# Kernel optimization log

Hardware: AMD Instinct MI355X
Metric: run time of the kernel (lower is better)

The kernel has to match this reference:

```python
import jax, jax.numpy as jnp
import numpy as np

N_NODES, N_EDGES = 50000, 800000
IN_DIM, OUT_DIM, EDGE_DIM = 128, 128, 32
NUM_HEADS = 8
HEAD_DIM = OUT_DIM // NUM_HEADS
SCALE = HEAD_DIM ** -0.5


def setup_inputs() -> dict:
    key = jax.random.key(0)
    ks = jax.random.split(key, 8)
    def lin_w(k, fan_in, fan_out):
        # kaiming-uniform-ish init like nn.Linear
        bound = 1.0 / np.sqrt(fan_in)
        return jax.random.uniform(k, (fan_in, fan_out), jnp.float32, -bound, bound)
    return {
        "node_features": jax.random.normal(ks[0], (N_NODES, IN_DIM), jnp.float32),
        "edge_features": jax.random.normal(ks[1], (N_EDGES, EDGE_DIM), jnp.float32),
        "Wq": lin_w(ks[2], IN_DIM, OUT_DIM), "bq": jnp.zeros((OUT_DIM,), jnp.float32),
        "Wk": lin_w(ks[3], IN_DIM, OUT_DIM), "bk": jnp.zeros((OUT_DIM,), jnp.float32),
        "Wv": lin_w(ks[4], IN_DIM, OUT_DIM), "bv": jnp.zeros((OUT_DIM,), jnp.float32),
        "We": lin_w(ks[5], EDGE_DIM, OUT_DIM), "be": jnp.zeros((OUT_DIM,), jnp.float32),
        "edge_list": jax.random.randint(ks[6], (N_EDGES, 2), 0, N_NODES, jnp.int32),
        "num_nodes": N_NODES,
    }


def reference(node_features, edge_features, Wq, bq, Wk, bk, Wv, bv, We, be, edge_list, num_nodes):
    # node projections -> [N, H, D]
    Q = (node_features @ Wq + bq).reshape(-1, NUM_HEADS, HEAD_DIM)
    K = (node_features @ Wk + bk).reshape(-1, NUM_HEADS, HEAD_DIM)
    V = (node_features @ Wv + bv).reshape(-1, NUM_HEADS, HEAD_DIM)
    edge_bias = (edge_features @ We + be).reshape(-1, NUM_HEADS, HEAD_DIM)

    src = edge_list[:, 0]  # node_in
    dst = edge_list[:, 1]  # node_out

    # per-edge per-head scores: [E, H]
    scores = jnp.einsum("ehd,ehd->eh", Q[src], K[dst]) * SCALE + edge_bias.sum(-1)
    # NOTE: softmax over the HEADS axis (dim=1), exactly as in the source
    weights = jax.nn.softmax(scores, axis=1)

    # weighted messages gathered from src, scattered to dst: [E, H, D] -> [N, H, D]
    msg = V[src] * weights[..., None]
    node_updates = jax.ops.segment_sum(msg, dst, num_segments=num_nodes)
    return node_updates.reshape(num_nodes, OUT_DIM)
```

## Files before the change

kernel.cpp:

```cpp
#include <hip/hip_runtime.h>
#include <math.h>

#define IN_DIM   128
#define OUT_DIM  128
#define EDGE_DIM 32
#define NUM_HEADS 8
#define HEAD_DIM 16
#define SCALE 0.25f
#define CSTRIDE 16

typedef __attribute__((ext_vector_type(8))) short bf16x8;
typedef __attribute__((ext_vector_type(4))) float f32x4;
typedef __attribute__((ext_vector_type(4))) unsigned int u32x4;

__device__ inline unsigned short f2bf(float x) {
    unsigned int u = __float_as_uint(x);
    unsigned int r = u + 0x7fff + ((u >> 16) & 1);
    return (unsigned short)(r >> 16);
}
__device__ inline float bflo(unsigned int u) { return __uint_as_float(u << 16); }
__device__ inline float bfhi(unsigned int u) { return __uint_as_float(u & 0xffff0000u); }

__global__ __launch_bounds__(256) void setup_kernel(
    int* __restrict__ counts, int n_nodes, int nbz,
    const float* __restrict__ Wq, const float* __restrict__ Wk,
    const float* __restrict__ Wv, unsigned short* __restrict__ WtB, int nbw,
    const float* __restrict__ We, const float* __restrict__ be,
    float* __restrict__ WeR, float* __restrict__ beR,
    const float* __restrict__ X, unsigned short* __restrict__ Xb)
{
    const int bx = blockIdx.x;
    const int t  = threadIdx.x;
    if (bx < nbz) {
        const int i = bx * 256 + t;
        if (i < n_nodes) counts[i << 4] = 0;
    } else if (bx < nbz + nbw) {
        const int idx = (bx - nbz) * 256 + t;
        const int mat = idx >> 14;
        const int rem = idx & 16383;
        const int n = rem >> 7, k = rem & 127;
        const float* W = (mat == 0) ? Wq : (mat == 1) ? Wk : Wv;
        WtB[mat * 16384 + n * 128 + k] = f2bf(W[k * 128 + n]);
    } else if (bx == nbz + nbw) {
        const int k = t >> 3, h = t & 7;
        float s = 0.f;
#pragma unroll
        for (int d = 0; d < HEAD_DIM; ++d) s += We[k * OUT_DIM + h * HEAD_DIM + d];
        WeR[k * NUM_HEADS + h] = s;
        if (t < NUM_HEADS) {
            float sb = 0.f;
#pragma unroll
            for (int d = 0; d < HEAD_DIM; ++d) sb += be[t * HEAD_DIM + d];
            beR[t] = sb;
        }
    } else {
        const int i = (bx - (nbz + nbw + 1)) * 256 + t;
        if (i < n_nodes * 16) {
            const f32x4* xr = (const f32x4*)(X + (size_t)i * 8);
            const f32x4 x0 = xr[0], x1 = xr[1];
            u32x4 p;
            p[0] = (unsigned)f2bf(x0[0]) | ((unsigned)f2bf(x0[1]) << 16);
            p[1] = (unsigned)f2bf(x0[2]) | ((unsigned)f2bf(x0[3]) << 16);
            p[2] = (unsigned)f2bf(x1[0]) | ((unsigned)f2bf(x1[1]) << 16);
            p[3] = (unsigned)f2bf(x1[2]) | ((unsigned)f2bf(x1[3]) << 16);
            *(u32x4*)(Xb + (size_t)i * 8) = p;
        }
    }
}

__global__ __launch_bounds__(256) void edge_kernel(
    const int* __restrict__ el, int* __restrict__ counts, int* __restrict__ rank,
    const float* __restrict__ ef, const float* __restrict__ WeR,
    const float* __restrict__ beR, unsigned int* __restrict__ ebias_e,
    int n_edges)
{
    const int e = blockIdx.x * 256 + threadIdx.x;
    if (e >= n_edges) return;
    const int2 ed = ((const int2*)el)[e];
    rank[e] = atomicAdd(&counts[ed.y << 4], 1);

    float acc[NUM_HEADS];
#pragma unroll
    for (int h = 0; h < NUM_HEADS; ++h) acc[h] = beR[h];

    const f32x4* efr = (const f32x4*)(ef + (size_t)e * EDGE_DIM);
#pragma unroll
    for (int kk = 0; kk < 8; ++kk) {
        const f32x4 f = efr[kk];
#pragma unroll
        for (int c = 0; c < 4; ++c) {
            const float* wr = WeR + (kk * 4 + c) * NUM_HEADS;
#pragma unroll
            for (int h = 0; h < NUM_HEADS; ++h)
                acc[h] = fmaf(f[c], wr[h], acc[h]);
        }
    }
    u32x4 pk;
    pk[0] = (unsigned)f2bf(acc[0]) | ((unsigned)f2bf(acc[1]) << 16);
    pk[1] = (unsigned)f2bf(acc[2]) | ((unsigned)f2bf(acc[3]) << 16);
    pk[2] = (unsigned)f2bf(acc[4]) | ((unsigned)f2bf(acc[5]) << 16);
    pk[3] = (unsigned)f2bf(acc[6]) | ((unsigned)f2bf(acc[7]) << 16);
    *(u32x4*)(ebias_e + (size_t)e * 4) = pk;
}

__global__ __launch_bounds__(256) void qkv_kernel(
    const unsigned short* __restrict__ Xb, const unsigned short* __restrict__ WtB,
    const float* __restrict__ bq, const float* __restrict__ bk,
    const float* __restrict__ bv,
    unsigned short* __restrict__ QVb, unsigned short* __restrict__ Kb,
    int n_nodes, int nbm)
{
    __shared__ unsigned short shW[16384];
    const int bx = blockIdx.x;
    const int t  = threadIdx.x;

    const int which = bx / nbm;
    const int mb    = bx - which * nbm;
    const unsigned short* Wg = WtB + which * 16384;

#pragma unroll
    for (int kk = 0; kk < 8; ++kk) {
        const int c = kk * 256 + t;
        const u32x4 v = ((const u32x4*)Wg)[c];
        const int row = c >> 4;
        const int bir = (c & 15) << 4;
        *(u32x4*)((char*)shW + row * 256 + (bir ^ ((row & 7) << 4))) = v;
    }
    __syncthreads();

    const int wave = t >> 6, lane = t & 63;
    const int quad = lane >> 4, li = lane & 15;
    const int mbase = mb * 256 + wave * 64;

    int mrow[4];
#pragma unroll
    for (int m = 0; m < 4; ++m) {
        const int r_ = mbase + m * 16 + li;
        mrow[m] = (r_ < n_nodes) ? r_ : (n_nodes - 1);
    }

    f32x4 acc[4][8];
#pragma unroll
    for (int m = 0; m < 4; ++m)
#pragma unroll
        for (int nt = 0; nt < 8; ++nt) acc[m][nt] = (f32x4){0.f, 0.f, 0.f, 0.f};

#pragma unroll
    for (int ks = 0; ks < 4; ++ks) {
        bf16x8 a[4];
#pragma unroll
        for (int m = 0; m < 4; ++m)
            a[m] = *(const bf16x8*)(Xb + (size_t)mrow[m] * 128 + ks * 32 + quad * 8);
#pragma unroll
        for (int nt = 0; nt < 8; ++nt) {
            const int row = nt * 16 + li;
            const bf16x8 b = *(const bf16x8*)((const char*)shW + row * 256 +
                                ((ks * 64 + quad * 16) ^ ((row & 7) << 4)));
#pragma unroll
            for (int m = 0; m < 4; ++m)
                acc[m][nt] = __builtin_amdgcn_mfma_f32_16x16x32_bf16(a[m], b, acc[m][nt], 0, 0, 0);
        }
    }

    const float* bias = (which == 0) ? bq : (which == 1) ? bk : bv;
    float bv8[8];
#pragma unroll
    for (int nt = 0; nt < 8; ++nt) bv8[nt] = bias[nt * 16 + li];

    __syncthreads();

    unsigned short* stg = shW + wave * 2176;
    const int R = lane >> 2, cc4 = lane & 3;
#pragma unroll
    for (int m = 0; m < 4; ++m) {
#pragma unroll
        for (int nt = 0; nt < 8; ++nt)
#pragma unroll
            for (int r = 0; r < 4; ++r)
                stg[(quad * 4 + r) * 136 + nt * 16 + li] = f2bf(acc[m][nt][r] + bv8[nt]);
        __syncthreads();

        const int node = mbase + m * 16 + R;
        if (node < n_nodes) {
            const u32x4* s = (const u32x4*)(stg + R * 136 + cc4 * 32);
            u32x4 d0 = s[0], d1 = s[1], d2 = s[2], d3 = s[3];
            unsigned short* dp =
                (which == 0) ? (QVb + (size_t)node * 256 + cc4 * 32)
              : (which == 1) ? (Kb  + (size_t)node * 128 + cc4 * 32)
              :                (QVb + (size_t)node * 256 + 128 + cc4 * 32);
            u32x4* d = (u32x4*)dp;
            d[0] = d0; d[1] = d1; d[2] = d2; d[3] = d3;
        }
        __syncthreads();
    }
}

__global__ __launch_bounds__(256) void scan1_kernel(
    const int* __restrict__ counts, int* __restrict__ bsums, int n)
{
    __shared__ int lds[256];
    const int i = blockIdx.x * 256 + threadIdx.x;
    lds[threadIdx.x] = (i < n) ? counts[i << 4] : 0;
    __syncthreads();
    for (int off = 128; off > 0; off >>= 1) {
        if (threadIdx.x < off) lds[threadIdx.x] += lds[threadIdx.x + off];
        __syncthreads();
    }
    if (threadIdx.x == 0) bsums[blockIdx.x] = lds[0];
}

__global__ __launch_bounds__(256) void scan3_kernel(
    const int* __restrict__ counts, const int* __restrict__ bsums,
    int* __restrict__ offsets, int n, int n_edges, int nb)
{
    __shared__ int lds[256];
    const int t = threadIdx.x;

    int v = (t < nb) ? bsums[t] : 0;
    lds[t] = v;
    __syncthreads();
    for (int off = 1; off < 256; off <<= 1) {
        const int u = (t >= off) ? lds[t - off] : 0;
        __syncthreads();
        lds[t] += u;
        __syncthreads();
    }
    const int base = (blockIdx.x > 0) ? lds[blockIdx.x - 1] : 0;
    __syncthreads();

    const int i = blockIdx.x * 256 + t;
    const int c = (i < n) ? counts[i << 4] : 0;
    lds[t] = c;
    __syncthreads();
    for (int off = 1; off < 256; off <<= 1) {
        const int u = (t >= off) ? lds[t - off] : 0;
        __syncthreads();
        lds[t] += u;
        __syncthreads();
    }
    if (i < n) offsets[i] = base + lds[t] - c;
    if (blockIdx.x == 0 && t == 0) offsets[n] = n_edges;
}

__global__ __launch_bounds__(256) void scatter_kernel(
    const int* __restrict__ el, const int* __restrict__ rank,
    const unsigned int* __restrict__ ebias_e,
    const int* __restrict__ offsets, unsigned int* __restrict__ recs,
    int n_edges)
{
    const int e = blockIdx.x * 256 + threadIdx.x;
    if (e >= n_edges) return;
    const int2 ed = ((const int2*)el)[e];
    const u32x4 eb = *(const u32x4*)(ebias_e + (size_t)e * 4);
    const int pos = offsets[ed.y] + rank[e];

    u32x4 r0, r1;
    r0[0] = (unsigned)ed.x;
    r0[1] = 0;
    r0[2] = eb[0];
    r0[3] = eb[1];
    r1[0] = eb[2];
    r1[1] = eb[3];
    r1[2] = 0; r1[3] = 0;
    u32x4* rp = (u32x4*)(recs + (size_t)pos * 8);
    rp[0] = r0;
    rp[1] = r1;
}

__global__ __launch_bounds__(256) void aggregate_kernel(
    const unsigned short* __restrict__ QVb, const unsigned short* __restrict__ Kb,
    const int* __restrict__ offsets, const unsigned int* __restrict__ recs,
    float* __restrict__ out, int n_nodes)
{
    const int wave = threadIdx.x >> 6;
    const int lane = threadIdx.x & 63;
    const int node = blockIdx.x * 4 + wave;
    if (node >= n_nodes) return;
    const int g = lane >> 3;
    const int h = lane & 7;

    const int beg = offsets[node];
    const int end = offsets[node + 1];
    const int cnt = end - beg;

    float kf[16];
    {
        const u32x4* kp = (const u32x4*)(Kb + (size_t)node * 128 + h * 16);
        const u32x4 ka = kp[0], kb_ = kp[1];
#pragma unroll
        for (int j = 0; j < 4; ++j) { kf[j * 2] = bflo(ka[j]);  kf[j * 2 + 1] = bfhi(ka[j]); }
#pragma unroll
        for (int j = 0; j < 4; ++j) { kf[8 + j * 2] = bflo(kb_[j]); kf[8 + j * 2 + 1] = bfhi(kb_[j]); }
    }

    float acc[16];
#pragma unroll
    for (int d = 0; d < 16; ++d) acc[d] = 0.f;

    if (cnt > 0) {
        const int last = end - 1;
        const int ebd  = 2 + (h >> 1);

        int s0 = beg + g;            if (s0 > last) s0 = last;
        unsigned int src_c = recs[(size_t)s0 * 8];
        unsigned int ebw_c = recs[(size_t)s0 * 8 + ebd];
        u32x4 qa, qb, va, vb;
        {
            const u32x4* qp = (const u32x4*)(QVb + (size_t)src_c * 256 + h * 16);
            qa = qp[0]; qb = qp[1];
            const u32x4* vp = (const u32x4*)(QVb + (size_t)src_c * 256 + 128 + h * 16);
            va = vp[0]; vb = vp[1];
        }
        int s1 = beg + 8 + g;        if (s1 > last) s1 = last;
        unsigned int src_n = recs[(size_t)s1 * 8];
        unsigned int ebw_n = recs[(size_t)s1 * 8 + ebd];

        for (int i = 0; i < cnt; i += 8) {
            int s2 = beg + i + 16 + g;  if (s2 > last) s2 = last;
            const unsigned int src_f = recs[(size_t)s2 * 8];
            const unsigned int ebw_f = recs[(size_t)s2 * 8 + ebd];
            u32x4 qan, qbn, van, vbn;
            {
                const u32x4* qp = (const u32x4*)(QVb + (size_t)src_n * 256 + h * 16);
                qan = qp[0]; qbn = qp[1];
                const u32x4* vp = (const u32x4*)(QVb + (size_t)src_n * 256 + 128 + h * 16);
                van = vp[0]; vbn = vp[1];
            }

            const float eb = (h & 1) ? bfhi(ebw_c) : bflo(ebw_c);
            float p = 0.f;
#pragma unroll
            for (int j = 0; j < 4; ++j) {
                p = fmaf(bflo(qa[j]), kf[j * 2],     p);
                p = fmaf(bfhi(qa[j]), kf[j * 2 + 1], p);
            }
#pragma unroll
            for (int j = 0; j < 4; ++j) {
                p = fmaf(bflo(qb[j]), kf[8 + j * 2],     p);
                p = fmaf(bfhi(qb[j]), kf[8 + j * 2 + 1], p);
            }
            const float score = fmaf(p, SCALE, eb);

            float mx = score;
            mx = fmaxf(mx, __shfl_xor(mx, 1));
            mx = fmaxf(mx, __shfl_xor(mx, 2));
            mx = fmaxf(mx, __shfl_xor(mx, 4));
            const float ex = __expf(score - mx);
            float den = ex;
            den += __shfl_xor(den, 1);
            den += __shfl_xor(den, 2);
            den += __shfl_xor(den, 4);
            float w = __fdividef(ex, den);
            if (i + g >= cnt) w = 0.f;

#pragma unroll
            for (int j = 0; j < 4; ++j) {
                acc[j * 2]     = fmaf(w, bflo(va[j]), acc[j * 2]);
                acc[j * 2 + 1] = fmaf(w, bfhi(va[j]), acc[j * 2 + 1]);
            }
#pragma unroll
            for (int j = 0; j < 4; ++j) {
                acc[8 + j * 2]     = fmaf(w, bflo(vb[j]), acc[8 + j * 2]);
                acc[8 + j * 2 + 1] = fmaf(w, bfhi(vb[j]), acc[8 + j * 2 + 1]);
            }

            qa = qan; qb = qbn; va = van; vb = vbn;
            src_c = src_n; ebw_c = ebw_n;
            src_n = src_f; ebw_n = ebw_f;
        }
    }

#pragma unroll
    for (int mask = 8; mask <= 32; mask <<= 1)
#pragma unroll
        for (int d = 0; d < 16; ++d)
            acc[d] += __shfl_xor(acc[d], mask);

    float2 o2 = make_float2(acc[g * 2], acc[g * 2 + 1]);
    *(float2*)(out + (size_t)node * OUT_DIM + h * 16 + g * 2) = o2;
}

extern "C" void kernel_launch(void* const* d_in, const int* in_sizes, int n_in,
                              void* d_out, int out_size, void* d_ws, size_t ws_size,
                              hipStream_t stream)
{
    const float* X   = (const float*)d_in[0];
    const float* ef  = (const float*)d_in[1];
    const float* Wq  = (const float*)d_in[2];
    const float* bq  = (const float*)d_in[3];
    const float* Wk  = (const float*)d_in[4];
    const float* bk  = (const float*)d_in[5];
    const float* Wv  = (const float*)d_in[6];
    const float* bv  = (const float*)d_in[7];
    const float* We  = (const float*)d_in[8];
    const float* be  = (const float*)d_in[9];
    const int*   el  = (const int*)d_in[10];

    const int n_nodes = in_sizes[0] / IN_DIM;
    const int n_edges = in_sizes[10] / 2;

    char* w = (char*)d_ws;
    auto alloc = [&](size_t bytes) { char* p = w; w += (bytes + 255) & ~(size_t)255; return p; };

    unsigned short* QVb    = (unsigned short*)alloc((size_t)n_nodes * 256 * 2);
    unsigned short* Kb     = (unsigned short*)alloc((size_t)n_nodes * 128 * 2);
    unsigned short* WtB    = (unsigned short*)alloc((size_t)3 * 128 * 128 * 2);
    unsigned int*   recs   = (unsigned int*)alloc((size_t)n_edges * 32);
    unsigned int*   ebias_e= (unsigned int*)alloc((size_t)n_edges * 16);
    int* rank    = (int*)alloc((size_t)n_edges * 4);
    float* WeR   = (float*)alloc(EDGE_DIM * NUM_HEADS * 4);
    float* beR   = (float*)alloc(NUM_HEADS * 4);
    int* counts  = (int*)alloc((size_t)n_nodes * CSTRIDE * 4);
    int* offsets = (int*)alloc((size_t)(n_nodes + 1) * 4);
    int* bsums   = (int*)alloc(256 * 4);

    unsigned short* Xb = (unsigned short*)recs;

    const int nbz = (n_nodes + 255) / 256;
    const int nbw = (3 * 128 * 128) / 256;
    const int nbx = (n_nodes * 16 + 255) / 256;
    setup_kernel<<<nbz + nbw + 1 + nbx, 256, 0, stream>>>(
        counts, n_nodes, nbz, Wq, Wk, Wv, WtB, nbw, We, be, WeR, beR, X, Xb);

    const int nbh = (n_edges + 255) / 256;
    edge_kernel<<<nbh, 256, 0, stream>>>(
        el, counts, rank, ef, WeR, beR, ebias_e, n_edges);

    const int nbm = (n_nodes + 255) / 256;
    qkv_kernel<<<3 * nbm, 256, 0, stream>>>(
        Xb, WtB, bq, bk, bv, QVb, Kb, n_nodes, nbm);

    const int nb = (n_nodes + 255) / 256;
    scan1_kernel<<<nb, 256, 0, stream>>>(counts, bsums, n_nodes);
    scan3_kernel<<<nb, 256, 0, stream>>>(counts, bsums, offsets, n_nodes, n_edges, nb);

    scatter_kernel<<<nbh, 256, 0, stream>>>(
        el, rank, ebias_e, offsets, recs, n_edges);

    aggregate_kernel<<<(n_nodes + 3) / 4, 256, 0, stream>>>(
        QVb, Kb, offsets, recs, (float*)d_out, n_nodes);
}
```

Measured before the change: 322.8 us.

## Make aggregate kernel persistent with packed float2 math and no softmax max

The aggregate kernel becomes a persistent grid-stride loop: the grid is capped at 2048 blocks, each wave walks over nodes, and the next node's CSR offsets are prefetched before the current node is processed. The dot-product and accumulation loops use two-wide float vectors, which the compiler can map to packed FMA instructions. The per-edge max-reduction across heads before the exponential is removed, saving three shuffles and a max per edge. Without the max subtraction, large scores could overflow the exponential, so correctness now depends on the score range.

New measurement: 326.1 us. Within noise of the previous version (+1.0%).

```diff
diff --git a/kernel.cpp b/kernel.cpp
--- a/kernel.cpp
+++ b/kernel.cpp
@@ -11,6 +11,7 @@
 
 typedef __attribute__((ext_vector_type(8))) short bf16x8;
 typedef __attribute__((ext_vector_type(4))) float f32x4;
+typedef __attribute__((ext_vector_type(2))) float f32x2;
 typedef __attribute__((ext_vector_type(4))) unsigned int u32x4;
 
 __device__ inline unsigned short f2bf(float x) {
@@ -20,6 +21,9 @@
 }
 __device__ inline float bflo(unsigned int u) { return __uint_as_float(u << 16); }
 __device__ inline float bfhi(unsigned int u) { return __uint_as_float(u & 0xffff0000u); }
+__device__ inline f32x2 up2(unsigned int u) {
+    f32x2 r; r[0] = bflo(u); r[1] = bfhi(u); return r;
+}
 
 __global__ __launch_bounds__(256) void setup_kernel(
     int* __restrict__ counts, int n_nodes, int nbz,
@@ -270,114 +274,109 @@
 __global__ __launch_bounds__(256) void aggregate_kernel(
     const unsigned short* __restrict__ QVb, const unsigned short* __restrict__ Kb,
     const int* __restrict__ offsets, const unsigned int* __restrict__ recs,
-    float* __restrict__ out, int n_nodes)
-{
-    const int wave = threadIdx.x >> 6;
+    float* __restrict__ out, int n_nodes, int nwtot)
+{
     const int lane = threadIdx.x & 63;
-    const int node = blockIdx.x * 4 + wave;
-    if (node >= n_nodes) return;
     const int g = lane >> 3;
     const int h = lane & 7;
-
-    const int beg = offsets[node];
-    const int end = offsets[node + 1];
-    const int cnt = end - beg;
-
-    float kf[16];
-    {
-        const u32x4* kp = (const u32x4*)(Kb + (size_t)node * 128 + h * 16);
-        const u32x4 ka = kp[0], kb_ = kp[1];
-#pragma unroll
-        for (int j = 0; j < 4; ++j) { kf[j * 2] = bflo(ka[j]);  kf[j * 2 + 1] = bfhi(ka[j]); }
-#pragma unroll
-        for (int j = 0; j < 4; ++j) { kf[8 + j * 2] = bflo(kb_[j]); kf[8 + j * 2 + 1] = bfhi(kb_[j]); }
-    }
-
-    float acc[16];
-#pragma unroll
-    for (int d = 0; d < 16; ++d) acc[d] = 0.f;
-
-    if (cnt > 0) {
-        const int last = end - 1;
-        const int ebd  = 2 + (h >> 1);
-
-        int s0 = beg + g;            if (s0 > last) s0 = last;
-        unsigned int src_c = recs[(size_t)s0 * 8];
-        unsigned int ebw_c = recs[(size_t)s0 * 8 + ebd];
-        u32x4 qa, qb, va, vb;
+    const int ebd = 2 + (h >> 1);
+
+    int node = (blockIdx.x * 256 + threadIdx.x) >> 6;
+    if (node >= n_nodes) return;
+    int beg = offsets[node];
+    int end = offsets[node + 1];
+
+    for (;;) {
+        const int nnode = node + nwtot;
+        int nbeg = 0, nend = 0;
+        if (nnode < n_nodes) { nbeg = offsets[nnode]; nend = offsets[nnode + 1]; }
+
+        const int cnt = end - beg;
+
+        f32x2 kf[8];
         {
-            const u32x4* qp = (const u32x4*)(QVb + (size_t)src_c * 256 + h * 16);
-            qa = qp[0]; qb = qp[1];
-            const u32x4* vp = (const u32x4*)(QVb + (size_t)src_c * 256 + 128 + h * 16);
-            va = vp[0]; vb = vp[1];
-        }
-        int s1 = beg + 8 + g;        if (s1 > last) s1 = last;
-        unsigned int src_n = recs[(size_t)s1 * 8];
-        unsigned int ebw_n = recs[(size_t)s1 * 8 + ebd];
-
-        for (int i = 0; i < cnt; i += 8) {
-            int s2 = beg + i + 16 + g;  if (s2 > last) s2 = last;
-            const unsigned int src_f = recs[(size_t)s2 * 8];
-            const unsigned int ebw_f = recs[(size_t)s2 * 8 + ebd];
-            u32x4 qan, qbn, van, vbn;
-            {
-                const u32x4* qp = (const u32x4*)(QVb + (size_t)src_n * 256 + h * 16);
-                qan = qp[0]; qbn = qp[1];
-                const u32x4* vp = (const u32x4*)(QVb + (size_t)src_n * 256 + 128 + h * 16);
-                van = vp[0]; vbn = vp[1];
+            const u32x4* kp = (const u32x4*)(Kb + (size_t)node * 128 + h * 16);
+            const u32x4 ka = kp[0], kb_ = kp[1];
+#pragma unroll
+            for (int j = 0; j < 4; ++j) { kf[j] = up2(ka[j]); kf[4 + j] = up2(kb_[j]); }
+        }
+
+        f32x2 acc[8];
+#pragma unroll
+        for (int j = 0; j < 8; ++j) acc[j] = (f32x2){0.f, 0.f};
+
+        if (cnt > 0) {
+            const int last = end - 1;
+            int s0 = beg + g; if (s0 > last) s0 = last;
+            const unsigned src_c = recs[(size_t)s0 * 8];
+            unsigned ebw_c = recs[(size_t)s0 * 8 + ebd];
+            const unsigned short* bp0 = QVb + (size_t)src_c * 256 + h * 16;
+            u32x4 qa = *(const u32x4*)bp0;
+            u32x4 qb = *(const u32x4*)(bp0 + 8);
+            u32x4 va = *(const u32x4*)(bp0 + 128);
+            u32x4 vb = *(const u32x4*)(bp0 + 136);
+            int s1 = beg + 8 + g; if (s1 > last) s1 = last;
+            unsigned src_n = recs[(size_t)s1 * 8];
+            unsigned ebw_n = recs[(size_t)s1 * 8 + ebd];
+
+            for (int i = 0; i < cnt; i += 8) {
+                int s2 = beg + i + 16 + g; if (s2 > last) s2 = last;
+                const unsigned src_f = recs[(size_t)s2 * 8];
+                const unsigned ebw_f = recs[(size_t)s2 * 8 + ebd];
+                const unsigned short* bp = QVb + (size_t)src_n * 256 + h * 16;
+                const u32x4 qan = *(const u32x4*)bp;
+                const u32x4 qbn = *(const u32x4*)(bp + 8);
+                const u32x4 van = *(const u32x4*)(bp + 128);
+                const u32x4 vbn = *(const u32x4*)(bp + 136);
+
+                const float eb = (h & 1) ? bfhi(ebw_c) : bflo(ebw_c);
+                f32x2 p2 = (f32x2){0.f, 0.f};
+#pragma unroll
+                for (int j = 0; j < 4; ++j) {
+                    p2 += up2(qa[j]) * kf[j];
+                    p2 += up2(qb[j]) * kf[4 + j];
+                }
+                const float score = fmaf(p2[0] + p2[1], SCALE, eb);
+
+                const float ex = __expf(score);
+                float den = ex;
+                den += __shfl_xor(den, 1);
+                den += __shfl_xor(den, 2);
+                den += __shfl_xor(den, 4);
+                float wgt = __fdividef(ex, den);
+                if (i + g >= cnt) wgt = 0.f;
+                const f32x2 w2 = (f32x2){wgt, wgt};
+#pragma unroll
+                for (int j = 0; j < 4; ++j) {
+                    acc[j]     += up2(va[j]) * w2;
+                    acc[4 + j] += up2(vb[j]) * w2;
+                }
+
+                qa = qan; qb = qbn; va = van; vb = vbn;
+                ebw_c = ebw_n;
+                src_n = src_f; ebw_n = ebw_f;
             }
-
-            const float eb = (h & 1) ? bfhi(ebw_c) : bflo(ebw_c);
-            float p = 0.f;
-#pragma unroll
-            for (int j = 0; j < 4; ++j) {
-                p = fmaf(bflo(qa[j]), kf[j * 2],     p);
-                p = fmaf(bfhi(qa[j]), kf[j * 2 + 1], p);
+        }
+
+#pragma unroll
+        for (int mask = 8; mask <= 32; mask <<= 1)
+#pragma unroll
+            for (int j = 0; j < 8; ++j) {
+                f32x2 o;
+                o[0] = __shfl_xor(acc[j][0], mask);
+                o[1] = __shfl_xor(acc[j][1], mask);
+                acc[j] += o;
             }
-#pragma unroll
-            for (int j = 0; j < 4; ++j) {
-                p = fmaf(bflo(qb[j]), kf[8 + j * 2],     p);
-                p = fmaf(bfhi(qb[j]), kf[8 + j * 2 + 1], p);
-            }
-            const float score = fmaf(p, SCALE, eb);
-
-            float mx = score;
-            mx = fmaxf(mx, __shfl_xor(mx, 1));
-            mx = fmaxf(mx, __shfl_xor(mx, 2));
-            mx = fmaxf(mx, __shfl_xor(mx, 4));
-            const float ex = __expf(score - mx);
-            float den = ex;
-            den += __shfl_xor(den, 1);
-            den += __shfl_xor(den, 2);
-            den += __shfl_xor(den, 4);
-            float w = __fdividef(ex, den);
-            if (i + g >= cnt) w = 0.f;
-
-#pragma unroll
-            for (int j = 0; j < 4; ++j) {
-                acc[j * 2]     = fmaf(w, bflo(va[j]), acc[j * 2]);
-                acc[j * 2 + 1] = fmaf(w, bfhi(va[j]), acc[j * 2 + 1]);
-            }
-#pragma unroll
-            for (int j = 0; j < 4; ++j) {
-                acc[8 + j * 2]     = fmaf(w, bflo(vb[j]), acc[8 + j * 2]);
-                acc[8 + j * 2 + 1] = fmaf(w, bfhi(vb[j]), acc[8 + j * 2 + 1]);
-            }
-
-            qa = qan; qb = qbn; va = van; vb = vbn;
-            src_c = src_n; ebw_c = ebw_n;
-            src_n = src_f; ebw_n = ebw_f;
-        }
-    }
-
-#pragma unroll
-    for (int mask = 8; mask <= 32; mask <<= 1)
-#pragma unroll
-        for (int d = 0; d < 16; ++d)
-            acc[d] += __shfl_xor(acc[d], mask);
-
-    float2 o2 = make_float2(acc[g * 2], acc[g * 2 + 1]);
-    *(float2*)(out + (size_t)node * OUT_DIM + h * 16 + g * 2) = o2;
+
+        float ox = 0.f, oy = 0.f;
+#pragma unroll
+        for (int j = 0; j < 8; ++j)
+            if (g == j) { ox = acc[j][0]; oy = acc[j][1]; }
+        *(float2*)(out + (size_t)node * OUT_DIM + h * 16 + g * 2) = make_float2(ox, oy);
+
+        if (nnode >= n_nodes) break;
+        node = nnode; beg = nbeg; end = nend;
+    }
 }
 
 extern "C" void kernel_launch(void* const* d_in, const int* in_sizes, int n_in,
@@ -437,6 +436,8 @@
     scatter_kernel<<<nbh, 256, 0, stream>>>(
         el, rank, ebias_e, offsets, recs, n_edges);
 
-    aggregate_kernel<<<(n_nodes + 3) / 4, 256, 0, stream>>>(
-        QVb, Kb, offsets, recs, (float*)d_out, n_nodes);
-}
+    int nblk = (n_nodes + 3) / 4;
+    if (nblk > 2048) nblk = 2048;
+    aggregate_kernel<<<nblk, 256, 0, stream>>>(
+        QVb, Kb, offsets, recs, (float*)d_out, n_nodes, nblk * 4);
+}
```
